# Kernel optimization log

Measured on AMD Instinct MI355X. Metric: run time of the kernel, lower is better.

The kernel has to match this reference:

```python
import jax, jax.numpy as jnp
import numpy as np

IN_F = 1024
OUT_F = 1024
GRID = 8
TOKENS = 8192


def setup_inputs() -> dict:
    key = jax.random.key(0)
    k_x, k_w, k_b, k_s = jax.random.split(key, 4)
    x = jax.random.normal(k_x, (TOKENS, IN_F), dtype=jnp.float32)
    # kaiming_uniform_(nonlinearity='linear'): bound = sqrt(3/fan_in)
    bound_w = float(np.sqrt(3.0 / IN_F))
    W = jax.random.uniform(k_w, (OUT_F, IN_F), minval=-bound_w, maxval=bound_w, dtype=jnp.float32)
    # nn.Linear default bias init: U(-1/sqrt(fan_in), 1/sqrt(fan_in))
    bound_b = float(1.0 / np.sqrt(IN_F))
    b = jax.random.uniform(k_b, (OUT_F,), minval=-bound_b, maxval=bound_b, dtype=jnp.float32)
    spline_weight = jax.random.uniform(k_s, (OUT_F, IN_F, GRID), minval=-0.1, maxval=0.1, dtype=jnp.float32)
    grid = jnp.linspace(-3.0, 3.0, GRID, dtype=jnp.float32)
    return {"x": x, "W": W, "b": b, "spline_weight": spline_weight, "grid": grid}


def reference(x, W, b, spline_weight, grid):
    grid_size = spline_weight.shape[-1]
    # base path: Linear(silu(x))
    base = jnp.einsum('ti,oi->to', jax.nn.silu(x), W) + b
    # RBF basis: [tokens, in_features, grid_size]
    denom = 2.0 / (grid_size - 1) + 1e-05
    basis = jnp.exp(-(((x[..., None] - grid) / denom) ** 2))
    spline = jnp.einsum('tig,oig->to', basis, spline_weight)
    return base + spline
```

## Files before the change

kernel.cpp:

```cpp
#include <hip/hip_runtime.h>
#include <hip/hip_bf16.h>

#define IN_F   1024
#define OUT_F  1024
#define GRID_N 8
#define TOKENS 8192
#define KTOT   9216
#define KHALF  4608
#define NTILE  72

typedef __attribute__((ext_vector_type(8))) short  bf16x8;
typedef __attribute__((ext_vector_type(4))) float  f32x4;

struct TrueT  { static constexpr bool value = true;  };
struct FalseT { static constexpr bool value = false; };

__device__ __forceinline__ unsigned int f2bf(float f) {
    union { float f; unsigned int u; } v; v.f = f;
    unsigned int r = v.u + 0x7fffu + ((v.u >> 16) & 1u);
    return r >> 16;
}

__global__ __launch_bounds__(256)
void prep_a_kernel(const float* __restrict__ x, const float* __restrict__ grid,
                   unsigned short* __restrict__ A)
{
    int idx = blockIdx.x * blockDim.x + threadIdx.x;
    int t = idx >> 10;
    int i = idx & 1023;
    float xv = x[idx];
    float sil = xv / (1.0f + __expf(-xv));
    A[(size_t)t * KTOT + i] = (unsigned short)f2bf(sil);

    const float invd = 1.0f / (2.0f / 7.0f + 1e-5f);
    unsigned int h[8];
    #pragma unroll
    for (int g = 0; g < 8; ++g) {
        float d = (xv - grid[g]) * invd;
        h[g] = f2bf(__expf(-d * d));
    }
    uint4 pk;
    pk.x = h[0] | (h[1] << 16);
    pk.y = h[2] | (h[3] << 16);
    pk.z = h[4] | (h[5] << 16);
    pk.w = h[6] | (h[7] << 16);
    *reinterpret_cast<uint4*>(&A[(size_t)t * KTOT + IN_F + (size_t)i * 8]) = pk;
}

__global__ __launch_bounds__(256)
void prep_b_kernel(const float* __restrict__ W, const float* __restrict__ spl,
                   unsigned short* __restrict__ B)
{
    int idx = blockIdx.x * blockDim.x + threadIdx.x;
    int o  = idx / (KTOT / 8);
    int c8 = idx - o * (KTOT / 8);
    const float* src = (c8 < IN_F / 8)
        ? (W   + (size_t)o * IN_F            + (size_t)c8 * 8)
        : (spl + (size_t)o * (IN_F * GRID_N) + (size_t)(c8 - IN_F / 8) * 8);
    const float4* s4 = reinterpret_cast<const float4*>(src);
    float4 lo = s4[0], hi = s4[1];
    uint4 pk;
    pk.x = f2bf(lo.x) | (f2bf(lo.y) << 16);
    pk.y = f2bf(lo.z) | (f2bf(lo.w) << 16);
    pk.z = f2bf(hi.x) | (f2bf(hi.y) << 16);
    pk.w = f2bf(hi.z) | (f2bf(hi.w) << 16);
    *reinterpret_cast<uint4*>(&B[(size_t)o * KTOT + (size_t)c8 * 8]) = pk;
}

#define GLOAD(src, dst) __builtin_amdgcn_global_load_lds( \
    (const __attribute__((address_space(1))) void*)(src),  \
    (__attribute__((address_space(3))) void*)(dst), 16, 0, 0)
#define SBAR()  __builtin_amdgcn_s_barrier()
#define SCH0()  __builtin_amdgcn_sched_barrier(0)
#define LGKM0() asm volatile("s_waitcnt lgkmcnt(0)" ::: "memory")
#define VMCNT_(n) asm volatile("s_waitcnt vmcnt(" #n ")" ::: "memory")

__global__ __launch_bounds__(512, 2)
void gemm_kan2(const unsigned short* __restrict__ A,
               const unsigned short* __restrict__ B,
               float* __restrict__ P, int rows)
{
    __shared__ char lds[131072];

    const int bid  = blockIdx.x;
    const int sk   = bid & 1;
    const int bn   = (bid >> 1) & 3;
    const int bm   = bid >> 3;
    const int tid  = threadIdx.x;
    const int wave = tid >> 6, lane = tid & 63;
    const int wr   = wave >> 2, wc = wave & 3;
    const int fr   = lane & 15, kg = lane >> 4;
    const int sw   = fr & 7;
    const int koff[2] = { (kg ^ sw) * 16, ((4 | kg) ^ sw) * 16 };
    const int k0 = sk * KHALF;

    const int trow = tid >> 3;
    const int ksrc = ((tid & 7) ^ (trow & 7)) * 8;
    const unsigned short* gA = A + (size_t)(bm * 256 + trow) * KTOT + k0 + ksrc;
    const unsigned short* gB = B + (size_t)(bn * 256 + trow) * KTOT + k0 + ksrc;
    const size_t R64 = (size_t)64 * KTOT;

    f32x4 acc[8][4];
    const f32x4 zero = {0.f, 0.f, 0.f, 0.f};
    #pragma unroll
    for (int m = 0; m < 8; ++m)
        #pragma unroll
        for (int n = 0; n < 4; ++n) acc[m][n] = zero;

    {
        char* d = lds + tid * 16;
        GLOAD(gA,           d);            GLOAD(gA + R64,     d + 8192);
        GLOAD(gB,           d + 32768);    GLOAD(gB + R64,     d + 40960);
        GLOAD(gB + 2 * R64, d + 49152);    GLOAD(gB + 3 * R64, d + 57344);
        GLOAD(gA + 2 * R64, d + 16384);    GLOAD(gA + 3 * R64, d + 24576);
        gA += 64; gB += 64;
    }
    VMCNT_(4); SBAR(); SCH0();

    const int aOff = (wr * 64 + fr) * 128;
    const int bOff = 32768 + (wc * 32 + fr) * 128;

    bf16x8 af[4][2], bf[2][2];
    int u = 0;

    auto tile = [&](auto stC) {
        constexpr bool ST = decltype(stC)::value;
        char* bufc = lds + (u & 1) * 65536;

        #pragma unroll
        for (int mi = 0; mi < 4; ++mi)
            #pragma unroll
            for (int ks = 0; ks < 2; ++ks)
                af[mi][ks] = *(const bf16x8*)(bufc + aOff + mi * 2048 + koff[ks]);
        #pragma unroll
        for (int ni = 0; ni < 2; ++ni)
            #pragma unroll
            for (int ks = 0; ks < 2; ++ks)
                bf[ni][ks] = *(const bf16x8*)(bufc + bOff + ni * 2048 + koff[ks]);
        if constexpr (ST) {
            char* d = lds + ((u & 1) ^ 1) * 65536 + tid * 16;
            GLOAD(gA,           d);            GLOAD(gA + R64,     d + 8192);
            GLOAD(gB,           d + 32768);    GLOAD(gB + R64,     d + 40960);
            GLOAD(gB + 2 * R64, d + 49152);    GLOAD(gB + 3 * R64, d + 57344);
            GLOAD(gA + 2 * R64, d + 16384);    GLOAD(gA + 3 * R64, d + 24576);
            VMCNT_(8);
        } else {
            VMCNT_(0);
        }
        SBAR(); SCH0(); LGKM0(); SCH0();
        __builtin_amdgcn_s_setprio(1);
        #pragma unroll
        for (int mi = 0; mi < 4; ++mi)
            #pragma unroll
            for (int ni = 0; ni < 2; ++ni)
                #pragma unroll
                for (int ks = 0; ks < 2; ++ks)
                    acc[mi][ni] = __builtin_amdgcn_mfma_f32_16x16x32_bf16(
                        af[mi][ks], bf[ni][ks], acc[mi][ni], 0, 0, 0);
        __builtin_amdgcn_s_setprio(0);
        SBAR(); SCH0();

        #pragma unroll
        for (int ni = 0; ni < 2; ++ni)
            #pragma unroll
            for (int ks = 0; ks < 2; ++ks)
                bf[ni][ks] = *(const bf16x8*)(bufc + bOff + 16384 + ni * 2048 + koff[ks]);
        SBAR(); SCH0(); LGKM0(); SCH0();
        __builtin_amdgcn_s_setprio(1);
        #pragma unroll
        for (int mi = 0; mi < 4; ++mi)
            #pragma unroll
            for (int ni = 0; ni < 2; ++ni)
                #pragma unroll
                for (int ks = 0; ks < 2; ++ks)
                    acc[mi][2 + ni] = __builtin_amdgcn_mfma_f32_16x16x32_bf16(
                        af[mi][ks], bf[ni][ks], acc[mi][2 + ni], 0, 0, 0);
        __builtin_amdgcn_s_setprio(0);
        SBAR(); SCH0();

        #pragma unroll
        for (int mi = 0; mi < 4; ++mi)
            #pragma unroll
            for (int ks = 0; ks < 2; ++ks)
                af[mi][ks] = *(const bf16x8*)(bufc + aOff + 16384 + mi * 2048 + koff[ks]);
        #pragma unroll
        for (int ni = 0; ni < 2; ++ni)
            #pragma unroll
            for (int ks = 0; ks < 2; ++ks)
                bf[ni][ks] = *(const bf16x8*)(bufc + bOff + ni * 2048 + koff[ks]);
        SBAR(); SCH0(); LGKM0(); SCH0();
        __builtin_amdgcn_s_setprio(1);
        #pragma unroll
        for (int mi = 0; mi < 4; ++mi)
            #pragma unroll
            for (int ni = 0; ni < 2; ++ni)
                #pragma unroll
                for (int ks = 0; ks < 2; ++ks)
                    acc[4 + mi][ni] = __builtin_amdgcn_mfma_f32_16x16x32_bf16(
                        af[mi][ks], bf[ni][ks], acc[4 + mi][ni], 0, 0, 0);
        __builtin_amdgcn_s_setprio(0);
        SBAR(); SCH0();

        #pragma unroll
        for (int ni = 0; ni < 2; ++ni)
            #pragma unroll
            for (int ks = 0; ks < 2; ++ks)
                bf[ni][ks] = *(const bf16x8*)(bufc + bOff + 16384 + ni * 2048 + koff[ks]);
        if constexpr (ST) {
            VMCNT_(4);
        }
        SBAR(); SCH0(); LGKM0(); SCH0();
        __builtin_amdgcn_s_setprio(1);
        #pragma unroll
        for (int mi = 0; mi < 4; ++mi)
            #pragma unroll
            for (int ni = 0; ni < 2; ++ni)
                #pragma unroll
                for (int ks = 0; ks < 2; ++ks)
                    acc[4 + mi][2 + ni] = __builtin_amdgcn_mfma_f32_16x16x32_bf16(
                        af[mi][ks], bf[ni][ks], acc[4 + mi][2 + ni], 0, 0, 0);
        __builtin_amdgcn_s_setprio(0);
        SBAR(); SCH0();

        if constexpr (ST) { gA += 64; gB += 64; }
    };

    for (u = 0; u < NTILE - 1; ++u) tile(TrueT{});
    tile(FalseT{});

    float* Pp = P + (size_t)sk * rows * OUT_F;
    const size_t orow0 = (size_t)bm * 256 + (size_t)wr * 64;
    const int    ocol0 = bn * 256 + wc * 32;
    #pragma unroll
    for (int n = 0; n < 4; ++n) {
        const int col = ocol0 + (n & 1) * 16 + (n >> 1) * 128 + fr;
        #pragma unroll
        for (int m = 0; m < 8; ++m) {
            const size_t r0 = orow0 + (m & 3) * 16 + (m >> 2) * 128 + kg * 4;
            #pragma unroll
            for (int j = 0; j < 4; ++j)
                Pp[(r0 + j) * OUT_F + col] = acc[m][n][j];
        }
    }
}

__global__ __launch_bounds__(256)
void reduce_kan(const float* __restrict__ P, const float* __restrict__ bias,
                float* __restrict__ out, int n4, int skStride4)
{
    const float4* p0 = (const float4*)P;
    const float4* p1 = p0 + skStride4;
    const float4* bv = (const float4*)bias;
    float4* o = (float4*)out;
    for (int i = blockIdx.x * blockDim.x + threadIdx.x; i < n4;
         i += gridDim.x * blockDim.x) {
        float4 a = p0[i], b = p1[i], c = bv[i & 255];
        float4 r;
        r.x = a.x + b.x + c.x;  r.y = a.y + b.y + c.y;
        r.z = a.z + b.z + c.z;  r.w = a.w + b.w + c.w;
        o[i] = r;
    }
}

extern "C" void kernel_launch(void* const* d_in, const int* in_sizes, int n_in,
                              void* d_out, int out_size, void* d_ws, size_t ws_size,
                              hipStream_t stream)
{
    const float* x    = (const float*)d_in[0];
    const float* W    = (const float*)d_in[1];
    const float* bias = (const float*)d_in[2];
    const float* spl  = (const float*)d_in[3];
    const float* grid = (const float*)d_in[4];
    float* out = (float*)d_out;

    unsigned short* Bw = (unsigned short*)d_ws;
    unsigned short* Aw = Bw + (size_t)OUT_F * KTOT;

    const size_t bBytes = (size_t)OUT_F * KTOT * 2;
    size_t avail = ws_size > bBytes ? ws_size - bBytes : 0;
    long maxRows = (long)(avail / 26624);
    int chunk = (maxRows >= TOKENS) ? TOKENS : (int)((maxRows / 256) * 256);
    if (chunk < 256) chunk = 256;
    float* Pp = (float*)(Aw + (size_t)chunk * KTOT);

    prep_b_kernel<<<(OUT_F * (KTOT / 8)) / 256, 256, 0, stream>>>(W, spl, Bw);

    for (int t0 = 0; t0 < TOKENS; t0 += chunk) {
        int rows = (TOKENS - t0 < chunk) ? (TOKENS - t0) : chunk;
        prep_a_kernel<<<(rows * IN_F) / 256, 256, 0, stream>>>(
            x + (size_t)t0 * IN_F, grid, Aw);
        gemm_kan2<<<(rows >> 8) * 8, 512, 0, stream>>>(Aw, Bw, Pp, rows);
        int n4 = rows * 256;
        int rblocks = (n4 + 255) / 256; if (rblocks > 2048) rblocks = 2048;
        reduce_kan<<<rblocks, 256, 0, stream>>>(
            Pp, bias, out + (size_t)t0 * OUT_F, n4, n4);
    }
}
```

Measured before the change: 215.9 us.

## Deepen GEMM prefetch to two tiles ahead and keep both B halves in registers

```diff
diff --git a/kernel.cpp b/kernel.cpp
--- a/kernel.cpp
+++ b/kernel.cpp
@@ -12,8 +12,7 @@
 typedef __attribute__((ext_vector_type(8))) short  bf16x8;
 typedef __attribute__((ext_vector_type(4))) float  f32x4;
 
-struct TrueT  { static constexpr bool value = true;  };
-struct FalseT { static constexpr bool value = false; };
+template<int M> struct ModeT { static constexpr int value = M; };
 
 __device__ __forceinline__ unsigned int f2bf(float f) {
     union { float f; unsigned int u; } v; v.f = f;
@@ -114,18 +113,25 @@
         GLOAD(gB + 2 * R64, d + 49152);    GLOAD(gB + 3 * R64, d + 57344);
         GLOAD(gA + 2 * R64, d + 16384);    GLOAD(gA + 3 * R64, d + 24576);
         gA += 64; gB += 64;
-    }
-    VMCNT_(4); SBAR(); SCH0();
+        d += 65536;
+        GLOAD(gA,           d);            GLOAD(gA + R64,     d + 8192);
+        GLOAD(gB,           d + 32768);    GLOAD(gB + R64,     d + 40960);
+        GLOAD(gB + 2 * R64, d + 49152);    GLOAD(gB + 3 * R64, d + 57344);
+        GLOAD(gA + 2 * R64, d + 16384);    GLOAD(gA + 3 * R64, d + 24576);
+        gA += 64; gB += 64;
+    }
+    VMCNT_(12); SBAR(); SCH0();
 
     const int aOff = (wr * 64 + fr) * 128;
     const int bOff = 32768 + (wc * 32 + fr) * 128;
 
-    bf16x8 af[4][2], bf[2][2];
+    bf16x8 af[4][2], bfLo[2][2], bfHi[2][2];
     int u = 0;
 
-    auto tile = [&](auto stC) {
-        constexpr bool ST = decltype(stC)::value;
+    auto tile = [&](auto mC) {
+        constexpr int MODE = decltype(mC)::value;
         char* bufc = lds + (u & 1) * 65536;
+        char* d    = bufc + tid * 16;
 
         #pragma unroll
         for (int mi = 0; mi < 4; ++mi)
@@ -136,16 +142,54 @@
         for (int ni = 0; ni < 2; ++ni)
             #pragma unroll
             for (int ks = 0; ks < 2; ++ks)
-                bf[ni][ks] = *(const bf16x8*)(bufc + bOff + ni * 2048 + koff[ks]);
-        if constexpr (ST) {
-            char* d = lds + ((u & 1) ^ 1) * 65536 + tid * 16;
-            GLOAD(gA,           d);            GLOAD(gA + R64,     d + 8192);
-            GLOAD(gB,           d + 32768);    GLOAD(gB + R64,     d + 40960);
-            GLOAD(gB + 2 * R64, d + 49152);    GLOAD(gB + 3 * R64, d + 57344);
-            GLOAD(gA + 2 * R64, d + 16384);    GLOAD(gA + 3 * R64, d + 24576);
-            VMCNT_(8);
-        } else {
-            VMCNT_(0);
+                bfLo[ni][ks] = *(const bf16x8*)(bufc + bOff + ni * 2048 + koff[ks]);
+        if constexpr (MODE == 0) { VMCNT_(10); }
+        else if constexpr (MODE == 1) { VMCNT_(10); }
+        else { VMCNT_(2); }
+        SBAR(); SCH0(); LGKM0(); SCH0();
+        __builtin_amdgcn_s_setprio(1);
+        #pragma unroll
+        for (int mi = 0; mi < 4; ++mi)
+            #pragma unroll
+            for (int ni = 0; ni < 2; ++ni)
+                #pragma unroll
+                for (int ks = 0; ks < 2; ++ks)
+                    acc[mi][ni] = __builtin_amdgcn_mfma_f32_16x16x32_bf16(
+                        af[mi][ks], bfLo[ni][ks], acc[mi][ni], 0, 0, 0);
+        __builtin_amdgcn_s_setprio(0);
+        SBAR(); SCH0();
+
+        #pragma unroll
+        for (int ni = 0; ni < 2; ++ni)
+            #pragma unroll
+            for (int ks = 0; ks < 2; ++ks)
+                bfHi[ni][ks] = *(const bf16x8*)(bufc + bOff + 16384 + ni * 2048 + koff[ks]);
+        if constexpr (MODE == 0) {
+            GLOAD(gA,       d);            GLOAD(gA + R64, d + 8192);
+            GLOAD(gB,       d + 32768);    GLOAD(gB + R64, d + 40960);
+            VMCNT_(12);
+        } else if constexpr (MODE == 1) { VMCNT_(8); }
+        else { VMCNT_(0); }
+        SBAR(); SCH0(); LGKM0(); SCH0();
+        __builtin_amdgcn_s_setprio(1);
+        #pragma unroll
+        for (int mi = 0; mi < 4; ++mi)
+            #pragma unroll
+            for (int ni = 0; ni < 2; ++ni)
+                #pragma unroll
+                for (int ks = 0; ks < 2; ++ks)
+                    acc[mi][2 + ni] = __builtin_amdgcn_mfma_f32_16x16x32_bf16(
+                        af[mi][ks], bfHi[ni][ks], acc[mi][2 + ni], 0, 0, 0);
+        __builtin_amdgcn_s_setprio(0);
+        SBAR(); SCH0();
+
+        #pragma unroll
+        for (int mi = 0; mi < 4; ++mi)
+            #pragma unroll
+            for (int ks = 0; ks < 2; ++ks)
+                af[mi][ks] = *(const bf16x8*)(bufc + aOff + 16384 + mi * 2048 + koff[ks]);
+        if constexpr (MODE == 0) {
+            GLOAD(gB + 2 * R64, d + 49152);  GLOAD(gB + 3 * R64, d + 57344);
         }
         SBAR(); SCH0(); LGKM0(); SCH0();
         __builtin_amdgcn_s_setprio(1);
@@ -155,40 +199,16 @@
             for (int ni = 0; ni < 2; ++ni)
                 #pragma unroll
                 for (int ks = 0; ks < 2; ++ks)
-                    acc[mi][ni] = __builtin_amdgcn_mfma_f32_16x16x32_bf16(
-                        af[mi][ks], bf[ni][ks], acc[mi][ni], 0, 0, 0);
-        __builtin_amdgcn_s_setprio(0);
-        SBAR(); SCH0();
-
-        #pragma unroll
-        for (int ni = 0; ni < 2; ++ni)
-            #pragma unroll
-            for (int ks = 0; ks < 2; ++ks)
-                bf[ni][ks] = *(const bf16x8*)(bufc + bOff + 16384 + ni * 2048 + koff[ks]);
-        SBAR(); SCH0(); LGKM0(); SCH0();
-        __builtin_amdgcn_s_setprio(1);
-        #pragma unroll
-        for (int mi = 0; mi < 4; ++mi)
-            #pragma unroll
-            for (int ni = 0; ni < 2; ++ni)
-                #pragma unroll
-                for (int ks = 0; ks < 2; ++ks)
-                    acc[mi][2 + ni] = __builtin_amdgcn_mfma_f32_16x16x32_bf16(
-                        af[mi][ks], bf[ni][ks], acc[mi][2 + ni], 0, 0, 0);
-        __builtin_amdgcn_s_setprio(0);
-        SBAR(); SCH0();
-
-        #pragma unroll
-        for (int mi = 0; mi < 4; ++mi)
-            #pragma unroll
-            for (int ks = 0; ks < 2; ++ks)
-                af[mi][ks] = *(const bf16x8*)(bufc + aOff + 16384 + mi * 2048 + koff[ks]);
-        #pragma unroll
-        for (int ni = 0; ni < 2; ++ni)
-            #pragma unroll
-            for (int ks = 0; ks < 2; ++ks)
-                bf[ni][ks] = *(const bf16x8*)(bufc + bOff + ni * 2048 + koff[ks]);
-        SBAR(); SCH0(); LGKM0(); SCH0();
+                    acc[4 + mi][2 + ni] = __builtin_amdgcn_mfma_f32_16x16x32_bf16(
+                        af[mi][ks], bfHi[ni][ks], acc[4 + mi][2 + ni], 0, 0, 0);
+        __builtin_amdgcn_s_setprio(0);
+        SBAR(); SCH0();
+
+        if constexpr (MODE == 0) {
+            GLOAD(gA + 2 * R64, d + 16384);  GLOAD(gA + 3 * R64, d + 24576);
+            VMCNT_(12);
+        } else if constexpr (MODE == 1) { VMCNT_(4); }
+        SBAR(); SCH0();
         __builtin_amdgcn_s_setprio(1);
         #pragma unroll
         for (int mi = 0; mi < 4; ++mi)
@@ -197,36 +217,17 @@
                 #pragma unroll
                 for (int ks = 0; ks < 2; ++ks)
                     acc[4 + mi][ni] = __builtin_amdgcn_mfma_f32_16x16x32_bf16(
-                        af[mi][ks], bf[ni][ks], acc[4 + mi][ni], 0, 0, 0);
-        __builtin_amdgcn_s_setprio(0);
-        SBAR(); SCH0();
-
-        #pragma unroll
-        for (int ni = 0; ni < 2; ++ni)
-            #pragma unroll
-            for (int ks = 0; ks < 2; ++ks)
-                bf[ni][ks] = *(const bf16x8*)(bufc + bOff + 16384 + ni * 2048 + koff[ks]);
-        if constexpr (ST) {
-            VMCNT_(4);
-        }
-        SBAR(); SCH0(); LGKM0(); SCH0();
-        __builtin_amdgcn_s_setprio(1);
-        #pragma unroll
-        for (int mi = 0; mi < 4; ++mi)
-            #pragma unroll
-            for (int ni = 0; ni < 2; ++ni)
-                #pragma unroll
-                for (int ks = 0; ks < 2; ++ks)
-                    acc[4 + mi][2 + ni] = __builtin_amdgcn_mfma_f32_16x16x32_bf16(
-                        af[mi][ks], bf[ni][ks], acc[4 + mi][2 + ni], 0, 0, 0);
-        __builtin_amdgcn_s_setprio(0);
-        SBAR(); SCH0();
-
-        if constexpr (ST) { gA += 64; gB += 64; }
+                        af[mi][ks], bfLo[ni][ks], acc[4 + mi][ni], 0, 0, 0);
+        __builtin_amdgcn_s_setprio(0);
+        SBAR(); SCH0();
+
+        if constexpr (MODE == 0) { gA += 64; gB += 64; }
     };
 
-    for (u = 0; u < NTILE - 1; ++u) tile(TrueT{});
-    tile(FalseT{});
+    for (u = 0; u < NTILE - 2; ++u) tile(ModeT<0>{});
+    tile(ModeT<1>{});
+    ++u;
+    tile(ModeT<2>{});
 
     float* Pp = P + (size_t)sk * rows * OUT_F;
     const size_t orow0 = (size_t)bm * 256 + (size_t)wr * 64;
```

After: 202.4 us. 6.2% less time.

## Fuse RBF basis generation into GEMM and drop split-K reduction

Applied to the files above, without the earlier changes.

```diff
diff --git a/kernel.cpp b/kernel.cpp
--- a/kernel.cpp
+++ b/kernel.cpp
@@ -3,17 +3,14 @@
 
 #define IN_F   1024
 #define OUT_F  1024
-#define GRID_N 8
 #define TOKENS 8192
 #define KTOT   9216
-#define KHALF  4608
-#define NTILE  72
+#define NTILE  144
 
 typedef __attribute__((ext_vector_type(8))) short  bf16x8;
 typedef __attribute__((ext_vector_type(4))) float  f32x4;
 
-struct TrueT  { static constexpr bool value = true;  };
-struct FalseT { static constexpr bool value = false; };
+template<int M> struct ModeT { static constexpr int value = M; };
 
 __device__ __forceinline__ unsigned int f2bf(float f) {
     union { float f; unsigned int u; } v; v.f = f;
@@ -22,29 +19,20 @@
 }
 
 __global__ __launch_bounds__(256)
-void prep_a_kernel(const float* __restrict__ x, const float* __restrict__ grid,
-                   unsigned short* __restrict__ A)
+void prep_a_lite(const float* __restrict__ x, unsigned short* __restrict__ siluA)
 {
     int idx = blockIdx.x * blockDim.x + threadIdx.x;
-    int t = idx >> 10;
-    int i = idx & 1023;
-    float xv = x[idx];
-    float sil = xv / (1.0f + __expf(-xv));
-    A[(size_t)t * KTOT + i] = (unsigned short)f2bf(sil);
-
-    const float invd = 1.0f / (2.0f / 7.0f + 1e-5f);
+    const float4* s = reinterpret_cast<const float4*>(x + (size_t)idx * 8);
+    float4 lo = s[0], hi = s[1];
+    float v[8] = {lo.x, lo.y, lo.z, lo.w, hi.x, hi.y, hi.z, hi.w};
     unsigned int h[8];
     #pragma unroll
-    for (int g = 0; g < 8; ++g) {
-        float d = (xv - grid[g]) * invd;
-        h[g] = f2bf(__expf(-d * d));
-    }
+    for (int j = 0; j < 8; ++j)
+        h[j] = f2bf(v[j] / (1.0f + __expf(-v[j])));
     uint4 pk;
-    pk.x = h[0] | (h[1] << 16);
-    pk.y = h[2] | (h[3] << 16);
-    pk.z = h[4] | (h[5] << 16);
-    pk.w = h[6] | (h[7] << 16);
-    *reinterpret_cast<uint4*>(&A[(size_t)t * KTOT + IN_F + (size_t)i * 8]) = pk;
+    pk.x = h[0] | (h[1] << 16);  pk.y = h[2] | (h[3] << 16);
+    pk.z = h[4] | (h[5] << 16);  pk.w = h[6] | (h[7] << 16);
+    reinterpret_cast<uint4*>(siluA)[idx] = pk;
 }
 
 __global__ __launch_bounds__(256)
@@ -55,8 +43,8 @@
     int o  = idx / (KTOT / 8);
     int c8 = idx - o * (KTOT / 8);
     const float* src = (c8 < IN_F / 8)
-        ? (W   + (size_t)o * IN_F            + (size_t)c8 * 8)
-        : (spl + (size_t)o * (IN_F * GRID_N) + (size_t)(c8 - IN_F / 8) * 8);
+        ? (W   + (size_t)o * IN_F     + (size_t)c8 * 8)
+        : (spl + (size_t)o * IN_F * 8 + (size_t)(c8 - IN_F / 8) * 8);
     const float4* s4 = reinterpret_cast<const float4*>(src);
     float4 lo = s4[0], hi = s4[1];
     uint4 pk;
@@ -73,79 +61,97 @@
 #define SBAR()  __builtin_amdgcn_s_barrier()
 #define SCH0()  __builtin_amdgcn_sched_barrier(0)
 #define LGKM0() asm volatile("s_waitcnt lgkmcnt(0)" ::: "memory")
-#define VMCNT_(n) asm volatile("s_waitcnt vmcnt(" #n ")" ::: "memory")
+#define VMC0()  asm volatile("s_waitcnt vmcnt(0)" ::: "memory")
 
 __global__ __launch_bounds__(512, 2)
-void gemm_kan2(const unsigned short* __restrict__ A,
-               const unsigned short* __restrict__ B,
-               float* __restrict__ P, int rows)
-{
-    __shared__ char lds[131072];
+void gemm_kan3(const float* __restrict__ x,
+               const unsigned short* __restrict__ siluA,
+               const unsigned short* __restrict__ Bw,
+               const float* __restrict__ grid,
+               const float* __restrict__ bias,
+               float* __restrict__ out)
+{
+    __shared__ uint4 lds4[98304 / 16];
+    char* lds = (char*)lds4;
 
     const int bid  = blockIdx.x;
-    const int sk   = bid & 1;
-    const int bn   = (bid >> 1) & 3;
-    const int bm   = bid >> 3;
+    const int bm   = bid & 31;
+    const int bn   = bid >> 5;
     const int tid  = threadIdx.x;
     const int wave = tid >> 6, lane = tid & 63;
     const int wr   = wave >> 2, wc = wave & 3;
     const int fr   = lane & 15, kg = lane >> 4;
     const int sw   = fr & 7;
     const int koff[2] = { (kg ^ sw) * 16, ((4 | kg) ^ sw) * 16 };
-    const int k0 = sk * KHALF;
+
+    const float invd  = 1.0f / (2.0f / 7.0f + 1e-5f);
+    const float invd2 = invd * 1.2011224087864498f;
+    float ng2[8];
+    #pragma unroll
+    for (int g = 0; g < 8; ++g) ng2[g] = -grid[g] * invd2;
 
     const int trow = tid >> 3;
-    const int ksrc = ((tid & 7) ^ (trow & 7)) * 8;
-    const unsigned short* gA = A + (size_t)(bm * 256 + trow) * KTOT + k0 + ksrc;
-    const unsigned short* gB = B + (size_t)(bn * 256 + trow) * KTOT + k0 + ksrc;
-    const size_t R64 = (size_t)64 * KTOT;
-
-    f32x4 acc[8][4];
+    const int gsw  = ((tid & 7) ^ (trow & 7)) * 8;
+    const unsigned short* gS = siluA + (size_t)(bm * 256 + trow) * 1024 + gsw;
+    const unsigned short* gB = Bw    + (size_t)(bn * 128 + trow) * 9216 + gsw;
+    const float*          xg = x     + (size_t)(bm * 256 + (tid >> 1)) * 1024
+                                     + (tid & 1) * 4;
+    const size_t R64S = (size_t)64 * 1024;
+    const size_t R64B = (size_t)64 * 9216;
+
+    f32x4 acc[8][2];
     const f32x4 zero = {0.f, 0.f, 0.f, 0.f};
     #pragma unroll
-    for (int m = 0; m < 8; ++m)
-        #pragma unroll
-        for (int n = 0; n < 4; ++n) acc[m][n] = zero;
+    for (int m = 0; m < 8; ++m) { acc[m][0] = zero; acc[m][1] = zero; }
 
     {
         char* d = lds + tid * 16;
-        GLOAD(gA,           d);            GLOAD(gA + R64,     d + 8192);
-        GLOAD(gB,           d + 32768);    GLOAD(gB + R64,     d + 40960);
-        GLOAD(gB + 2 * R64, d + 49152);    GLOAD(gB + 3 * R64, d + 57344);
-        GLOAD(gA + 2 * R64, d + 16384);    GLOAD(gA + 3 * R64, d + 24576);
-        gA += 64; gB += 64;
+        GLOAD(gS,            d);
+        GLOAD(gS + R64S,     d + 8192);
+        GLOAD(gS + 2 * R64S, d + 16384);
+        GLOAD(gS + 3 * R64S, d + 24576);
+        GLOAD(gB,            d + 65536);
+        GLOAD(gB + R64B,     d + 65536 + 8192);
+        gS += 64; gB += 64;
     }
-    VMCNT_(4); SBAR(); SCH0();
-
-    const int aOff = (wr * 64 + fr) * 128;
-    const int bOff = 32768 + (wc * 32 + fr) * 128;
+    VMC0(); SBAR(); SCH0();
+
+    const int aOff = (wr * 128 + fr) * 128;
+    const int bOff = (wc * 32 + fr) * 128;
 
     bf16x8 af[4][2], bf[2][2];
     int u = 0;
 
-    auto tile = [&](auto stC) {
-        constexpr bool ST = decltype(stC)::value;
-        char* bufc = lds + (u & 1) * 65536;
+    auto tile = [&](auto mC) {
+        constexpr int NEXT = decltype(mC)::value;
+        char* bufA = lds + (u & 1) * 32768;
+        char* bufB = lds + 65536 + (u & 1) * 16384;
+        char* dAn  = lds + ((u + 1) & 1) * 32768 + tid * 16;
+        char* dBn  = lds + 65536 + ((u + 1) & 1) * 16384 + tid * 16;
 
         #pragma unroll
         for (int mi = 0; mi < 4; ++mi)
             #pragma unroll
             for (int ks = 0; ks < 2; ++ks)
-                af[mi][ks] = *(const bf16x8*)(bufc + aOff + mi * 2048 + koff[ks]);
+                af[mi][ks] = *(const bf16x8*)(bufA + aOff + mi * 2048 + koff[ks]);
         #pragma unroll
         for (int ni = 0; ni < 2; ++ni)
             #pragma unroll
             for (int ks = 0; ks < 2; ++ks)
-                bf[ni][ks] = *(const bf16x8*)(bufc + bOff + ni * 2048 + koff[ks]);
-        if constexpr (ST) {
-            char* d = lds + ((u & 1) ^ 1) * 65536 + tid * 16;
-            GLOAD(gA,           d);            GLOAD(gA + R64,     d + 8192);
-            GLOAD(gB,           d + 32768);    GLOAD(gB + R64,     d + 40960);
-            GLOAD(gB + 2 * R64, d + 49152);    GLOAD(gB + 3 * R64, d + 57344);
-            GLOAD(gA + 2 * R64, d + 16384);    GLOAD(gA + 3 * R64, d + 24576);
-            VMCNT_(8);
-        } else {
-            VMCNT_(0);
+                bf[ni][ks] = *(const bf16x8*)(bufB + bOff + ni * 2048 + koff[ks]);
+        float4 xq = {0.f, 0.f, 0.f, 0.f};
+        if constexpr (NEXT == 0) {
+            GLOAD(gS,            dAn);
+            GLOAD(gS + R64S,     dAn + 8192);
+            GLOAD(gS + 2 * R64S, dAn + 16384);
+            GLOAD(gS + 3 * R64S, dAn + 24576);
+        }
+        if constexpr (NEXT == 1) {
+            xq = *reinterpret_cast<const float4*>(xg);
+        }
+        if constexpr (NEXT <= 1) {
+            GLOAD(gB,        dBn);
+            GLOAD(gB + R64B, dBn + 8192);
         }
         SBAR(); SCH0(); LGKM0(); SCH0();
         __builtin_amdgcn_s_setprio(1);
@@ -161,33 +167,10 @@
         SBAR(); SCH0();
 
         #pragma unroll
-        for (int ni = 0; ni < 2; ++ni)
+        for (int mi = 0; mi < 4; ++mi)
             #pragma unroll
             for (int ks = 0; ks < 2; ++ks)
-                bf[ni][ks] = *(const bf16x8*)(bufc + bOff + 16384 + ni * 2048 + koff[ks]);
-        SBAR(); SCH0(); LGKM0(); SCH0();
-        __builtin_amdgcn_s_setprio(1);
-        #pragma unroll
-        for (int mi = 0; mi < 4; ++mi)
-            #pragma unroll
-            for (int ni = 0; ni < 2; ++ni)
-                #pragma unroll
-                for (int ks = 0; ks < 2; ++ks)
-                    acc[mi][2 + ni] = __builtin_amdgcn_mfma_f32_16x16x32_bf16(
-                        af[mi][ks], bf[ni][ks], acc[mi][2 + ni], 0, 0, 0);
-        __builtin_amdgcn_s_setprio(0);
-        SBAR(); SCH0();
-
-        #pragma unroll
-        for (int mi = 0; mi < 4; ++mi)
-            #pragma unroll
-            for (int ks = 0; ks < 2; ++ks)
-                af[mi][ks] = *(const bf16x8*)(bufc + aOff + 16384 + mi * 2048 + koff[ks]);
-        #pragma unroll
-        for (int ni = 0; ni < 2; ++ni)
-            #pragma unroll
-            for (int ks = 0; ks < 2; ++ks)
-                bf[ni][ks] = *(const bf16x8*)(bufc + bOff + ni * 2048 + koff[ks]);
+                af[mi][ks] = *(const bf16x8*)(bufA + aOff + 8192 + mi * 2048 + koff[ks]);
         SBAR(); SCH0(); LGKM0(); SCH0();
         __builtin_amdgcn_s_setprio(1);
         #pragma unroll
@@ -199,66 +182,59 @@
                     acc[4 + mi][ni] = __builtin_amdgcn_mfma_f32_16x16x32_bf16(
                         af[mi][ks], bf[ni][ks], acc[4 + mi][ni], 0, 0, 0);
         __builtin_amdgcn_s_setprio(0);
-        SBAR(); SCH0();
-
-        #pragma unroll
-        for (int ni = 0; ni < 2; ++ni)
-            #pragma unroll
-            for (int ks = 0; ks < 2; ++ks)
-                bf[ni][ks] = *(const bf16x8*)(bufc + bOff + 16384 + ni * 2048 + koff[ks]);
-        if constexpr (ST) {
-            VMCNT_(4);
-        }
-        SBAR(); SCH0(); LGKM0(); SCH0();
-        __builtin_amdgcn_s_setprio(1);
-        #pragma unroll
-        for (int mi = 0; mi < 4; ++mi)
-            #pragma unroll
-            for (int ni = 0; ni < 2; ++ni)
-                #pragma unroll
-                for (int ks = 0; ks < 2; ++ks)
-                    acc[4 + mi][2 + ni] = __builtin_amdgcn_mfma_f32_16x16x32_bf16(
-                        af[mi][ks], bf[ni][ks], acc[4 + mi][2 + ni], 0, 0, 0);
-        __builtin_amdgcn_s_setprio(0);
-        SBAR(); SCH0();
-
-        if constexpr (ST) { gA += 64; gB += 64; }
+        if constexpr (NEXT == 1) {
+            const int   r   = tid >> 1;
+            const int   ib  = 4 * (tid & 1);
+            char* wbase = lds + ((u + 1) & 1) * 32768 + r * 128;
+            float xa[4] = {xq.x, xq.y, xq.z, xq.w};
+            #pragma unroll
+            for (int q = 0; q < 4; ++q) {
+                float e[8];
+                #pragma unroll
+                for (int g = 0; g < 8; ++g) {
+                    float t = fmaf(xa[q], invd2, ng2[g]);
+                    float a = -t * t;
+                    asm("v_exp_f32 %0, %1" : "=v"(e[g]) : "v"(a));
+                }
+                unsigned int pk[4];
+                #pragma unroll
+                for (int p = 0; p < 4; ++p) {
+                    __hip_bfloat162 h =
+                        __float22bfloat162_rn(float2{e[2 * p], e[2 * p + 1]});
+                    pk[p] = *reinterpret_cast<unsigned int*>(&h);
+                }
+                *reinterpret_cast<uint4*>(
+                    wbase + (((ib + q) ^ (r & 7)) * 16)) =
+                    make_uint4(pk[0], pk[1], pk[2], pk[3]);
+            }
+        }
+        if constexpr (NEXT <= 1) {
+            LGKM0();
+            VMC0();
+        }
+        SCH0(); SBAR(); SCH0();
+
+        if constexpr (NEXT == 0) { gS += 64; gB += 64; }
+        if constexpr (NEXT == 1) { xg += 8;  gB += 64; }
     };
 
-    for (u = 0; u < NTILE - 1; ++u) tile(TrueT{});
-    tile(FalseT{});
-
-    float* Pp = P + (size_t)sk * rows * OUT_F;
-    const size_t orow0 = (size_t)bm * 256 + (size_t)wr * 64;
-    const int    ocol0 = bn * 256 + wc * 32;
-    #pragma unroll
-    for (int n = 0; n < 4; ++n) {
-        const int col = ocol0 + (n & 1) * 16 + (n >> 1) * 128 + fr;
+    for (u = 0; u < 15; ++u)     tile(ModeT<0>{});
+    for (; u < NTILE - 1; ++u)   tile(ModeT<1>{});
+    tile(ModeT<2>{});
+
+    const size_t orow0 = (size_t)bm * 256 + (size_t)wr * 128;
+    const int    ocol0 = bn * 128 + wc * 32;
+    #pragma unroll
+    for (int n = 0; n < 2; ++n) {
+        const int col = ocol0 + n * 16 + fr;
+        const float bv = bias[col];
         #pragma unroll
         for (int m = 0; m < 8; ++m) {
-            const size_t r0 = orow0 + (m & 3) * 16 + (m >> 2) * 128 + kg * 4;
+            const size_t r0 = orow0 + (m >> 2) * 64 + (m & 3) * 16 + kg * 4;
             #pragma unroll
             for (int j = 0; j < 4; ++j)
-                Pp[(r0 + j) * OUT_F + col] = acc[m][n][j];
-        }
-    }
-}
-
-__global__ __launch_bounds__(256)
-void reduce_kan(const float* __restrict__ P, const float* __restrict__ bias,
-                float* __restrict__ out, int n4, int skStride4)
-{
-    const float4* p0 = (const float4*)P;
-    const float4* p1 = p0 + skStride4;
-    const float4* bv = (const float4*)bias;
-    float4* o = (float4*)out;
-    for (int i = blockIdx.x * blockDim.x + threadIdx.x; i < n4;
-         i += gridDim.x * blockDim.x) {
-        float4 a = p0[i], b = p1[i], c = bv[i & 255];
-        float4 r;
-        r.x = a.x + b.x + c.x;  r.y = a.y + b.y + c.y;
-        r.z = a.z + b.z + c.z;  r.w = a.w + b.w + c.w;
-        o[i] = r;
+                out[(r0 + j) * OUT_F + col] = acc[m][n][j] + bv;
+        }
     }
 }
 
@@ -273,26 +249,10 @@
     const float* grid = (const float*)d_in[4];
     float* out = (float*)d_out;
 
-    unsigned short* Bw = (unsigned short*)d_ws;
-    unsigned short* Aw = Bw + (size_t)OUT_F * KTOT;
-
-    const size_t bBytes = (size_t)OUT_F * KTOT * 2;
-    size_t avail = ws_size > bBytes ? ws_size - bBytes : 0;
-    long maxRows = (long)(avail / 26624);
-    int chunk = (maxRows >= TOKENS) ? TOKENS : (int)((maxRows / 256) * 256);
-    if (chunk < 256) chunk = 256;
-    float* Pp = (float*)(Aw + (size_t)chunk * KTOT);
+    unsigned short* Bw    = (unsigned short*)d_ws;
+    unsigned short* siluA = Bw + (size_t)OUT_F * KTOT;
 
     prep_b_kernel<<<(OUT_F * (KTOT / 8)) / 256, 256, 0, stream>>>(W, spl, Bw);
-
-    for (int t0 = 0; t0 < TOKENS; t0 += chunk) {
-        int rows = (TOKENS - t0 < chunk) ? (TOKENS - t0) : chunk;
-        prep_a_kernel<<<(rows * IN_F) / 256, 256, 0, stream>>>(
-            x + (size_t)t0 * IN_F, grid, Aw);
-        gemm_kan2<<<(rows >> 8) * 8, 512, 0, stream>>>(Aw, Bw, Pp, rows);
-        int n4 = rows * 256;
-        int rblocks = (n4 + 255) / 256; if (rblocks > 2048) rblocks = 2048;
-        reduce_kan<<<rblocks, 256, 0, stream>>>(
-            Pp, bias, out + (size_t)t0 * OUT_F, n4, n4);
-    }
-}
+    prep_a_lite<<<(TOKENS * IN_F / 8) / 256, 256, 0, stream>>>(x, siluA);
+    gemm_kan3<<<256, 512, 0, stream>>>(x, siluA, Bw, grid, bias, out);
+}
```

Measured after the change: 233.3 us. 1.08x slower.
